# Kernel optimization log

Hardware: AMD Instinct MI355X
Metric: run time of the kernel (lower is better)

Reference implementation:

```python
import jax, jax.numpy as jnp
import numpy as np


def setup_inputs() -> dict:
    key = jax.random.key(0)
    k1, k2, k3, k4 = jax.random.split(key, 4)
    N, F, E = 100000, 128, 1600000
    Fo = F // 2
    x = jax.random.normal(k1, (N, F), dtype=jnp.float32)
    edge_index = jax.random.randint(k2, (2, E), 0, N, dtype=jnp.int32)
    W_conv = jax.random.normal(k3, (Fo, F), dtype=jnp.float32) * (1.0 / np.sqrt(F))
    b_conv = jnp.zeros((Fo,), dtype=jnp.float32)
    W_lin = jax.random.normal(k4, (1, Fo), dtype=jnp.float32) * (1.0 / np.sqrt(Fo))
    b_lin = jnp.zeros((1,), dtype=jnp.float32)
    return {"x": x, "edge_index": edge_index, "W_conv": W_conv,
            "b_conv": b_conv, "W_lin": W_lin, "b_lin": b_lin}


def gcn_conv(x, edge_index, W_conv, b_conv):
    # PyG GCNConv: add self-loops, symmetric normalization, x@W.T, scatter-add, + bias
    N = x.shape[0]
    loops = jnp.arange(N, dtype=edge_index.dtype)
    src = jnp.concatenate([edge_index[0], loops])  # message sources
    dst = jnp.concatenate([edge_index[1], loops])  # aggregation targets
    h = x @ W_conv.T  # [N, Fo]
    deg = jax.ops.segment_sum(jnp.ones_like(dst, dtype=h.dtype), dst, num_segments=N)
    dinv = jnp.where(deg > 0, jax.lax.rsqrt(deg), 0.0)
    norm = dinv[src] * dinv[dst]  # [E+N]
    msg = h[src] * norm[:, None]  # [E+N, Fo] -- dominant memory traffic
    agg = jax.ops.segment_sum(msg, dst, num_segments=N)
    return agg + b_conv


def reference(x, edge_index, W_conv, b_conv, W_lin, b_lin):
    h = gcn_conv(x, edge_index, W_conv, b_conv)
    h = jax.nn.relu(h)
    logits = h @ W_lin.T + b_lin  # [N, 1]
    return jax.nn.sigmoid(logits)
```

## Files before the change

### kernel.cpp

```cpp
#include <hip/hip_runtime.h>
#include <hip/hip_bf16.h>
#include <math.h>

#define F_IN   128
#define F_OUT  64
#define CHUNK  5120
#define MAXB   512

typedef short bf16x8 __attribute__((ext_vector_type(8)));
typedef float f32x4  __attribute__((ext_vector_type(4)));

__device__ __forceinline__ unsigned short f2bf(float f) {
    union { float f; unsigned int i; } c; c.f = f;
    unsigned int r = c.i + 0x7FFFu + ((c.i >> 16) & 1u);
    return (unsigned short)(r >> 16);
}
__device__ __forceinline__ unsigned int pk2bf(float a, float b) {
    __hip_bfloat162 p = __float22bfloat162_rn(make_float2(a, b));
    union { __hip_bfloat162 h; unsigned int u; } c; c.h = p; return c.u;
}
__device__ __forceinline__ float u_lo(unsigned int u) {
    union { unsigned int i; float f; } c; c.i = u << 16; return c.f;
}
__device__ __forceinline__ float u_hi(unsigned int u) {
    union { unsigned int i; float f; } c; c.i = u & 0xFFFF0000u; return c.f;
}

__global__ __launch_bounds__(256) void k_hist(
    const int* __restrict__ dst, int E, int* __restrict__ M, int NBLK, int NBC) {
    __shared__ int hist[MAXB];
    for (int c = threadIdx.x; c < MAXB; c += 256) hist[c] = 0;
    __syncthreads();
    int e0 = blockIdx.x * CHUNK;
    int e1 = min(E, e0 + CHUNK);
    for (int e = e0 + threadIdx.x; e < e1; e += 256)
        atomicAdd(&hist[dst[e] >> 8], 1);
    __syncthreads();
    for (int c = threadIdx.x; c < NBC; c += 256)
        M[c * NBLK + blockIdx.x] = hist[c];
}

__global__ void k_scan1(const int* __restrict__ M, int* __restrict__ tmp,
                        int* __restrict__ bsum, int S) {
    __shared__ int sh[256];
    int i = blockIdx.x * 256 + threadIdx.x;
    int v = (i < S) ? M[i] : 0;
    sh[threadIdx.x] = v;
    __syncthreads();
    for (int off = 1; off < 256; off <<= 1) {
        int t = (threadIdx.x >= off) ? sh[threadIdx.x - off] : 0;
        __syncthreads();
        sh[threadIdx.x] += t;
        __syncthreads();
    }
    if (i < S) tmp[i] = sh[threadIdx.x];
    if (threadIdx.x == 255) bsum[blockIdx.x] = sh[255];
}

__global__ void k_scan2(int* __restrict__ bsum, int NB1) {
    __shared__ int sh[512];
    int v = (threadIdx.x < NB1) ? bsum[threadIdx.x] : 0;
    sh[threadIdx.x] = v;
    __syncthreads();
    for (int off = 1; off < 512; off <<= 1) {
        int t = (threadIdx.x >= off) ? sh[threadIdx.x - off] : 0;
        __syncthreads();
        sh[threadIdx.x] += t;
        __syncthreads();
    }
    if (threadIdx.x < NB1) bsum[threadIdx.x] = sh[threadIdx.x] - v;
}

__global__ void k_scan3(int* __restrict__ M, const int* __restrict__ tmp,
                        const int* __restrict__ bsum, int* __restrict__ bucketOff,
                        int S, int NBLK, int NBC, int E) {
    int i = blockIdx.x * 256 + threadIdx.x;
    if (i < S) {
        int orig = M[i];
        int o = tmp[i] - orig + bsum[blockIdx.x];
        M[i] = o;
        if (i % NBLK == 0) bucketOff[i / NBLK] = o;
    }
    if (i == 0) bucketOff[NBC] = E;
}

__global__ __launch_bounds__(256) void k_scatter(
    const int* __restrict__ src, const int* __restrict__ dst, int E,
    const int* __restrict__ M, int NBLK, int NBC, unsigned int* __restrict__ entries) {
    __shared__ int cur[MAXB];
    for (int c = threadIdx.x; c < NBC; c += 256)
        cur[c] = M[c * NBLK + blockIdx.x];
    __syncthreads();
    int e0 = blockIdx.x * CHUNK;
    int e1 = min(E, e0 + CHUNK);
    for (int e = e0 + threadIdx.x; e < e1; e += 256) {
        int d = dst[e];
        int s = src[e];
        int p = atomicAdd(&cur[d >> 8], 1);
        entries[p] = ((unsigned int)(d & 255) << 24) | (unsigned int)s;
    }
}

__global__ __launch_bounds__(256) void k_sort(
    const unsigned int* __restrict__ entries, const int* __restrict__ bucketOff,
    int* __restrict__ offsets, int* __restrict__ deg,
    unsigned int* __restrict__ srcs, int N) {
    __shared__ int hist[256];
    __shared__ int curs[256];
    const int tid = threadIdx.x;
    const int b = blockIdx.x;
    const int start = bucketOff[b];
    const int end   = bucketOff[b + 1];

    hist[tid] = 0;
    __syncthreads();
    for (int i = start + tid; i < end; i += 256)
        atomicAdd(&hist[entries[i] >> 24], 1);
    __syncthreads();

    int cntv = hist[tid];
    curs[tid] = cntv;
    __syncthreads();
    for (int off = 1; off < 256; off <<= 1) {
        int t = (tid >= off) ? curs[tid - off] : 0;
        __syncthreads();
        curs[tid] += t;
        __syncthreads();
    }
    int excl = curs[tid] - cntv;
    int d = (b << 8) + tid;
    if (d < N) { offsets[d] = start + excl; deg[d] = cntv; }
    __syncthreads();
    curs[tid] = start + excl;
    __syncthreads();

    for (int i = start + tid; i < end; i += 256) {
        unsigned int v = entries[i];
        int p = atomicAdd(&curs[v >> 24], 1);
        srcs[p] = (v & 0xFFFFFFu) << 7;
    }
}

__global__ __launch_bounds__(256) void k_gemm(
    const float* __restrict__ x, const float* __restrict__ W,
    const int* __restrict__ deg, unsigned short* __restrict__ g, int N) {
    __shared__ unsigned short xs[64 * F_IN];
    __shared__ unsigned short Wsh[F_OUT * F_IN];
    __shared__ float dinvs[64];

    const int tid  = threadIdx.x;
    const int row0 = blockIdx.x * 64;

    {
        const float4* W4 = (const float4*)W;
        #pragma unroll
        for (int t = 0; t < 8; ++t) {
            int idx = t * 256 + tid;
            float4 v = W4[idx];
            uint2 u = make_uint2(pk2bf(v.x, v.y), pk2bf(v.z, v.w));
            *(uint2*)&Wsh[idx * 4] = u;
        }
    }
    {
        const float4* x4 = (const float4*)x;
        #pragma unroll
        for (int t = 0; t < 8; ++t) {
            int idx = t * 256 + tid;
            int r = idx >> 5;
            int grow = row0 + r;
            float4 v = make_float4(0.f, 0.f, 0.f, 0.f);
            if (grow < N) v = x4[(size_t)grow * 32 + (idx & 31)];
            uint2 u = make_uint2(pk2bf(v.x, v.y), pk2bf(v.z, v.w));
            *(uint2*)&xs[idx * 4] = u;
        }
    }
    if (tid < 64) {
        int grow = row0 + tid;
        float dv = 1.0f;
        if (grow < N) dv = rsqrtf((float)deg[grow] + 1.0f);
        dinvs[tid] = dv;
    }
    __syncthreads();

    const int lane = tid & 63;
    const int wave = tid >> 6;
    const int m = lane & 15;
    const int q = lane >> 4;
    const int r0 = wave * 16;

    bf16x8 a[4];
    #pragma unroll
    for (int ks = 0; ks < 4; ++ks)
        a[ks] = *(const bf16x8*)&xs[(r0 + m) * F_IN + ks * 32 + q * 8];

    f32x4 acc[4] = {{0,0,0,0},{0,0,0,0},{0,0,0,0},{0,0,0,0}};
    #pragma unroll
    for (int ct = 0; ct < 4; ++ct) {
        #pragma unroll
        for (int ks = 0; ks < 4; ++ks) {
            bf16x8 b = *(const bf16x8*)&Wsh[(ct * 16 + m) * F_IN + ks * 32 + q * 8];
            acc[ct] = __builtin_amdgcn_mfma_f32_16x16x32_bf16(a[ks], b, acc[ct], 0, 0, 0);
        }
    }

    float dv[4];
    #pragma unroll
    for (int reg = 0; reg < 4; ++reg)
        dv[reg] = dinvs[r0 + q * 4 + reg];
    #pragma unroll
    for (int ct = 0; ct < 4; ++ct) {
        #pragma unroll
        for (int reg = 0; reg < 4; ++reg) {
            int grow = row0 + r0 + q * 4 + reg;
            if (grow <= N)
                g[(size_t)grow * F_OUT + ct * 16 + m] = f2bf(acc[ct][reg] * dv[reg]);
        }
    }
}

__global__ __launch_bounds__(256) void k_pull(
    const unsigned short* __restrict__ g, const int* __restrict__ offsets,
    const int* __restrict__ deg, const unsigned int* __restrict__ srcs,
    const float* __restrict__ b_conv, const float* __restrict__ W_lin,
    const float* __restrict__ b_lin, float* __restrict__ out, int N) {
    const int lane   = threadIdx.x & 63;
    const int li     = lane & 31;
    const int half   = lane >> 5;
    const int wave   = (blockIdx.x * blockDim.x + threadIdx.x) >> 6;
    const int nwaves = (gridDim.x * blockDim.x) >> 6;

    const float2 wl = ((const float2*)W_lin)[li];
    const float2 bb = ((const float2*)b_conv)[li];
    const float  bl = b_lin[0];
    const char* gb = (const char*)g;
    const unsigned int lioff = ((unsigned int)li) << 2;
    const unsigned int sentb = ((unsigned int)N) << 7;

    for (int i = wave; i < N; i += nwaves) {
        int e0 = __builtin_amdgcn_readfirstlane(offsets[i]);
        int dg = __builtin_amdgcn_readfirstlane(deg[i]);
        int full = dg >> 4;
        int rem  = dg & 15;

        unsigned int us = *(const unsigned int*)(gb + ((((unsigned int)i) << 7) | lioff));
        float2 acc;
        acc.x = half ? 0.f : u_lo(us);
        acc.y = half ? 0.f : u_hi(us);

        const unsigned int* sp = srcs + e0 + half;
        for (int it = 0; it < full; ++it) {
            unsigned int off[8];
            #pragma unroll
            for (int t = 0; t < 8; ++t)
                off[t] = sp[2 * t];
            unsigned int u[8];
            #pragma unroll
            for (int t = 0; t < 8; ++t)
                u[t] = *(const unsigned int*)(gb + (size_t)(off[t] | lioff));
            #pragma unroll
            for (int t = 0; t < 8; ++t) {
                acc.x += u_lo(u[t]);
                acc.y += u_hi(u[t]);
            }
            sp += 16;
        }
        if (rem) {
            unsigned int off[8];
            #pragma unroll
            for (int t = 0; t < 8; ++t) {
                unsigned int o = sp[2 * t];
                off[t] = (2 * t + half < rem) ? o : sentb;
            }
            unsigned int u[8];
            #pragma unroll
            for (int t = 0; t < 8; ++t)
                u[t] = *(const unsigned int*)(gb + (size_t)(off[t] | lioff));
            #pragma unroll
            for (int t = 0; t < 8; ++t) {
                acc.x += u_lo(u[t]);
                acc.y += u_hi(u[t]);
            }
        }

        acc.x += __shfl_xor(acc.x, 32, 64);
        acc.y += __shfl_xor(acc.y, 32, 64);

        float dinv = rsqrtf((float)dg + 1.0f);
        float r0 = fmaxf(acc.x * dinv + bb.x, 0.f);
        float r1 = fmaxf(acc.y * dinv + bb.y, 0.f);
        float t = r0 * wl.x + r1 * wl.y;
        #pragma unroll
        for (int off = 32; off > 0; off >>= 1)
            t += __shfl_down(t, off, 64);
        if (lane == 0)
            out[i] = 1.0f / (1.0f + expf(-(0.5f * t + bl)));
    }
}

extern "C" void kernel_launch(void* const* d_in, const int* in_sizes, int n_in,
                              void* d_out, int out_size, void* d_ws, size_t ws_size,
                              hipStream_t stream) {
    const float* x      = (const float*)d_in[0];
    const int*   ei     = (const int*)d_in[1];
    const float* W_conv = (const float*)d_in[2];
    const float* b_conv = (const float*)d_in[3];
    const float* W_lin  = (const float*)d_in[4];
    const float* b_lin  = (const float*)d_in[5];

    const int N = in_sizes[0] / F_IN;
    const int E = in_sizes[1] / 2;
    const int* src = ei;
    const int* dst = ei + E;
    float* out = (float*)d_out;

    const int NBC  = (N + 255) >> 8;
    const int NBLK = (E + CHUNK - 1) / CHUNK;
    const int S    = NBC * NBLK;
    const int NB1  = (S + 255) / 256;

    const int Na = (N + 256) & ~255;
    const int Sa = (S + 256) & ~255;
    const int Ea = (E + 255) & ~255;

    int* M         = (int*)d_ws;
    int* tmp       = M + Sa;
    int* bsum      = tmp + Sa;
    int* bucketOff = bsum + 512;
    int* offsets   = bucketOff + (MAXB + 256);
    int* deg       = offsets + Na;
    unsigned int* entries = (unsigned int*)(deg + Na);
    unsigned int* srcs    = (unsigned int*)(entries + Ea);
    unsigned short* g = (unsigned short*)(srcs + Ea + 256);

    k_hist   <<<NBLK, 256, 0, stream>>>(dst, E, M, NBLK, NBC);
    k_scan1  <<<NB1, 256, 0, stream>>>(M, tmp, bsum, S);
    k_scan2  <<<1, 512, 0, stream>>>(bsum, NB1);
    k_scan3  <<<NB1, 256, 0, stream>>>(M, tmp, bsum, bucketOff, S, NBLK, NBC, E);
    k_scatter<<<NBLK, 256, 0, stream>>>(src, dst, E, M, NBLK, NBC, entries);
    k_sort   <<<NBC, 256, 0, stream>>>(entries, bucketOff, offsets, deg, srcs, N);
    k_gemm   <<<(N + 64) / 64, 256, 0, stream>>>(x, W_conv, deg, g, N);
    k_pull   <<<4096, 256, 0, stream>>>(g, offsets, deg, srcs, b_conv, W_lin, b_lin, out, N);
}
```

Baseline: 188.2 us.

## Gather 8-byte rows with 4 edges per wave, pack offset/degree, unroll scatter loops

```diff
diff --git a/kernel.cpp b/kernel.cpp
--- a/kernel.cpp
+++ b/kernel.cpp
@@ -33,6 +33,7 @@
     __syncthreads();
     int e0 = blockIdx.x * CHUNK;
     int e1 = min(E, e0 + CHUNK);
+    #pragma unroll 4
     for (int e = e0 + threadIdx.x; e < e1; e += 256)
         atomicAdd(&hist[dst[e] >> 8], 1);
     __syncthreads();
@@ -93,6 +94,7 @@
     __syncthreads();
     int e0 = blockIdx.x * CHUNK;
     int e1 = min(E, e0 + CHUNK);
+    #pragma unroll 4
     for (int e = e0 + threadIdx.x; e < e1; e += 256) {
         int d = dst[e];
         int s = src[e];
@@ -103,8 +105,7 @@
 
 __global__ __launch_bounds__(256) void k_sort(
     const unsigned int* __restrict__ entries, const int* __restrict__ bucketOff,
-    int* __restrict__ offsets, int* __restrict__ deg,
-    unsigned int* __restrict__ srcs, int N) {
+    int2* __restrict__ od, unsigned int* __restrict__ srcs, int N) {
     __shared__ int hist[256];
     __shared__ int curs[256];
     const int tid = threadIdx.x;
@@ -129,7 +130,7 @@
     }
     int excl = curs[tid] - cntv;
     int d = (b << 8) + tid;
-    if (d < N) { offsets[d] = start + excl; deg[d] = cntv; }
+    if (d < N) od[d] = make_int2(start + excl, cntv);
     __syncthreads();
     curs[tid] = start + excl;
     __syncthreads();
@@ -143,7 +144,7 @@
 
 __global__ __launch_bounds__(256) void k_gemm(
     const float* __restrict__ x, const float* __restrict__ W,
-    const int* __restrict__ deg, unsigned short* __restrict__ g, int N) {
+    const int2* __restrict__ od, unsigned short* __restrict__ g, int N) {
     __shared__ unsigned short xs[64 * F_IN];
     __shared__ unsigned short Wsh[F_OUT * F_IN];
     __shared__ float dinvs[64];
@@ -177,7 +178,7 @@
     if (tid < 64) {
         int grow = row0 + tid;
         float dv = 1.0f;
-        if (grow < N) dv = rsqrtf((float)deg[grow] + 1.0f);
+        if (grow < N) dv = rsqrtf((float)od[grow].y + 1.0f);
         dinvs[tid] = dv;
     }
     __syncthreads();
@@ -219,81 +220,91 @@
 }
 
 __global__ __launch_bounds__(256) void k_pull(
-    const unsigned short* __restrict__ g, const int* __restrict__ offsets,
-    const int* __restrict__ deg, const unsigned int* __restrict__ srcs,
+    const unsigned short* __restrict__ g, const int2* __restrict__ od,
+    const unsigned int* __restrict__ srcs,
     const float* __restrict__ b_conv, const float* __restrict__ W_lin,
     const float* __restrict__ b_lin, float* __restrict__ out, int N) {
-    const int lane   = threadIdx.x & 63;
-    const int li     = lane & 31;
-    const int half   = lane >> 5;
+    const int lane = threadIdx.x & 63;
+    const int li   = lane & 15;
+    const int grp  = lane >> 4;
     const int wave   = (blockIdx.x * blockDim.x + threadIdx.x) >> 6;
     const int nwaves = (gridDim.x * blockDim.x) >> 6;
 
-    const float2 wl = ((const float2*)W_lin)[li];
-    const float2 bb = ((const float2*)b_conv)[li];
+    const float4 wl = ((const float4*)W_lin)[li];
+    const float4 bb = ((const float4*)b_conv)[li];
     const float  bl = b_lin[0];
     const char* gb = (const char*)g;
-    const unsigned int lioff = ((unsigned int)li) << 2;
+    const unsigned int lioff = ((unsigned int)li) << 3;
     const unsigned int sentb = ((unsigned int)N) << 7;
 
     for (int i = wave; i < N; i += nwaves) {
-        int e0 = __builtin_amdgcn_readfirstlane(offsets[i]);
-        int dg = __builtin_amdgcn_readfirstlane(deg[i]);
+        int2 odv = od[i];
+        int e0 = __builtin_amdgcn_readfirstlane(odv.x);
+        int dg = __builtin_amdgcn_readfirstlane(odv.y);
         int full = dg >> 4;
         int rem  = dg & 15;
 
-        unsigned int us = *(const unsigned int*)(gb + ((((unsigned int)i) << 7) | lioff));
-        float2 acc;
-        acc.x = half ? 0.f : u_lo(us);
-        acc.y = half ? 0.f : u_hi(us);
-
-        const unsigned int* sp = srcs + e0 + half;
+        uint2 us = *(const uint2*)(gb + ((((unsigned int)i) << 7) | lioff));
+        float4 acc;
+        acc.x = grp ? 0.f : u_lo(us.x);
+        acc.y = grp ? 0.f : u_hi(us.x);
+        acc.z = grp ? 0.f : u_lo(us.y);
+        acc.w = grp ? 0.f : u_hi(us.y);
+
+        const unsigned int* sp = srcs + e0 + grp;
         for (int it = 0; it < full; ++it) {
-            unsigned int off[8];
-            #pragma unroll
-            for (int t = 0; t < 8; ++t)
-                off[t] = sp[2 * t];
-            unsigned int u[8];
-            #pragma unroll
-            for (int t = 0; t < 8; ++t)
-                u[t] = *(const unsigned int*)(gb + (size_t)(off[t] | lioff));
-            #pragma unroll
-            for (int t = 0; t < 8; ++t) {
-                acc.x += u_lo(u[t]);
-                acc.y += u_hi(u[t]);
+            unsigned int off[4];
+            #pragma unroll
+            for (int t = 0; t < 4; ++t)
+                off[t] = sp[4 * t];
+            uint2 u[4];
+            #pragma unroll
+            for (int t = 0; t < 4; ++t)
+                u[t] = *(const uint2*)(gb + (size_t)(off[t] | lioff));
+            #pragma unroll
+            for (int t = 0; t < 4; ++t) {
+                acc.x += u_lo(u[t].x); acc.y += u_hi(u[t].x);
+                acc.z += u_lo(u[t].y); acc.w += u_hi(u[t].y);
             }
             sp += 16;
         }
         if (rem) {
-            unsigned int off[8];
-            #pragma unroll
-            for (int t = 0; t < 8; ++t) {
-                unsigned int o = sp[2 * t];
-                off[t] = (2 * t + half < rem) ? o : sentb;
+            unsigned int off[4];
+            #pragma unroll
+            for (int t = 0; t < 4; ++t) {
+                unsigned int o = sp[4 * t];
+                off[t] = (4 * t + grp < rem) ? o : sentb;
             }
-            unsigned int u[8];
-            #pragma unroll
-            for (int t = 0; t < 8; ++t)
-                u[t] = *(const unsigned int*)(gb + (size_t)(off[t] | lioff));
-            #pragma unroll
-            for (int t = 0; t < 8; ++t) {
-                acc.x += u_lo(u[t]);
-                acc.y += u_hi(u[t]);
+            uint2 u[4];
+            #pragma unroll
+            for (int t = 0; t < 4; ++t)
+                u[t] = *(const uint2*)(gb + (size_t)(off[t] | lioff));
+            #pragma unroll
+            for (int t = 0; t < 4; ++t) {
+                acc.x += u_lo(u[t].x); acc.y += u_hi(u[t].x);
+                acc.z += u_lo(u[t].y); acc.w += u_hi(u[t].y);
             }
         }
 
-        acc.x += __shfl_xor(acc.x, 32, 64);
-        acc.y += __shfl_xor(acc.y, 32, 64);
+        #pragma unroll
+        for (int m = 16; m <= 32; m <<= 1) {
+            acc.x += __shfl_xor(acc.x, m, 64);
+            acc.y += __shfl_xor(acc.y, m, 64);
+            acc.z += __shfl_xor(acc.z, m, 64);
+            acc.w += __shfl_xor(acc.w, m, 64);
+        }
 
         float dinv = rsqrtf((float)dg + 1.0f);
         float r0 = fmaxf(acc.x * dinv + bb.x, 0.f);
         float r1 = fmaxf(acc.y * dinv + bb.y, 0.f);
-        float t = r0 * wl.x + r1 * wl.y;
-        #pragma unroll
-        for (int off = 32; off > 0; off >>= 1)
-            t += __shfl_down(t, off, 64);
+        float r2 = fmaxf(acc.z * dinv + bb.z, 0.f);
+        float r3 = fmaxf(acc.w * dinv + bb.w, 0.f);
+        float t = r0 * wl.x + r1 * wl.y + r2 * wl.z + r3 * wl.w;
+        #pragma unroll
+        for (int m = 1; m <= 8; m <<= 1)
+            t += __shfl_xor(t, m, 64);
         if (lane == 0)
-            out[i] = 1.0f / (1.0f + expf(-(0.5f * t + bl)));
+            out[i] = 1.0f / (1.0f + expf(-(t + bl)));
     }
 }
 
@@ -326,9 +337,8 @@
     int* tmp       = M + Sa;
     int* bsum      = tmp + Sa;
     int* bucketOff = bsum + 512;
-    int* offsets   = bucketOff + (MAXB + 256);
-    int* deg       = offsets + Na;
-    unsigned int* entries = (unsigned int*)(deg + Na);
+    int2* od       = (int2*)(bucketOff + (MAXB + 256));
+    unsigned int* entries = (unsigned int*)((int*)od + 2 * Na);
     unsigned int* srcs    = (unsigned int*)(entries + Ea);
     unsigned short* g = (unsigned short*)(srcs + Ea + 256);
 
@@ -337,7 +347,7 @@
     k_scan2  <<<1, 512, 0, stream>>>(bsum, NB1);
     k_scan3  <<<NB1, 256, 0, stream>>>(M, tmp, bsum, bucketOff, S, NBLK, NBC, E);
     k_scatter<<<NBLK, 256, 0, stream>>>(src, dst, E, M, NBLK, NBC, entries);
-    k_sort   <<<NBC, 256, 0, stream>>>(entries, bucketOff, offsets, deg, srcs, N);
-    k_gemm   <<<(N + 64) / 64, 256, 0, stream>>>(x, W_conv, deg, g, N);
-    k_pull   <<<4096, 256, 0, stream>>>(g, offsets, deg, srcs, b_conv, W_lin, b_lin, out, N);
-}
+    k_sort   <<<NBC, 256, 0, stream>>>(entries, bucketOff, od, srcs, N);
+    k_gemm   <<<(N + 64) / 64, 256, 0, stream>>>(x, W_conv, od, g, N);
+    k_pull   <<<4096, 256, 0, stream>>>(g, od, srcs, b_conv, W_lin, b_lin, out, N);
+}
```

Measured after the change: 188.2 us. Within noise of the previous version (+0.0%).
